# Kernel tuning notes

Measured on AMD Instinct MI355X. Metric: run time of the kernel, lower is better.

Reference implementation:

```python
import jax, jax.numpy as jnp
import numpy as np

N = 100000   # nodes
E = 3200000  # edges
D = 128      # in_channels
H = 128      # subhiddens
O = 128      # out_channels
S = 2048     # subgraphs
EPS = 1e-5


def _glorot(k, shape):
    lim = np.sqrt(6.0 / (shape[0] + shape[1])).astype(np.float32)
    return jax.random.uniform(k, shape, jnp.float32, -lim, lim)


def setup_inputs() -> dict:
    key = jax.random.key(0)
    ks = jax.random.split(key, 8)
    x = jax.random.normal(ks[0], (N, D), jnp.float32)
    edge_index = jax.random.randint(ks[1], (2, E), 0, N, dtype=jnp.int32)
    node_to_subgraph = jnp.sort(jax.random.randint(ks[2], (N,), 0, S, dtype=jnp.int32))
    return {
        "x": x,
        "edge_index": edge_index,
        "node_to_subgraph": node_to_subgraph,
        "W1": _glorot(ks[3], (D, H)), "b1": jnp.zeros((H,), jnp.float32),
        "g1": jnp.ones((H,), jnp.float32), "be1": jnp.zeros((H,), jnp.float32),
        "W2": _glorot(ks[4], (H, H)), "b2": jnp.zeros((H,), jnp.float32),
        "g2": jnp.ones((H,), jnp.float32), "be2": jnp.zeros((H,), jnp.float32),
        "W3": _glorot(ks[5], (H, O)), "b3": jnp.zeros((O,), jnp.float32),
    }


def _gcn_conv(x, W, b, row, col, norm):
    # PyG GCNConv: out[col] += norm * (x @ W)[row], then + bias.
    xw = x @ W                                    # [N+?, d] -> [N, d_out]
    msg = xw[row] * norm[:, None]                 # gather over source nodes
    out = jax.ops.segment_sum(msg, col, num_segments=N)
    return out + b


def _bn_relu(x, g, be):
    # BatchNorm1d (training-mode batch stats, biased var) + ReLU
    mean = jnp.mean(x, axis=0)
    var = jnp.mean(jnp.square(x - mean), axis=0)
    return jax.nn.relu((x - mean) * jax.lax.rsqrt(var + EPS) * g + be)


def reference(x, edge_index, node_to_subgraph, W1, b1, g1, be1, W2, b2, g2, be2, W3, b3):
    # GCN symmetric norm with self-loops, shared across the 3 convs.
    loops = jnp.arange(N, dtype=edge_index.dtype)
    row = jnp.concatenate([edge_index[0], loops])  # source
    col = jnp.concatenate([edge_index[1], loops])  # target (aggregation)
    deg = jax.ops.segment_sum(jnp.ones_like(col, dtype=x.dtype), col, num_segments=N)
    dinv = jnp.where(deg > 0, jax.lax.rsqrt(deg), 0.0)
    norm = dinv[row] * dinv[col]

    h1 = _bn_relu(_gcn_conv(x, W1, b1, row, col, norm), g1, be1)   # dropout is no-op in eval
    h2 = _bn_relu(_gcn_conv(h1, W2, b2, row, col, norm), g2, be2)
    h3 = jax.nn.relu(_gcn_conv(h2, W3, b3, row, col, norm))

    cat = jnp.concatenate([h1, h2, h3], axis=-1)                   # [N, 2H+O]
    return jax.ops.segment_max(cat, node_to_subgraph, num_segments=S)  # gmp -> [S, 2H+O]
```

## Files before the change

### kernel.cpp

```cpp
#include <hip/hip_runtime.h>
#include <hip/hip_fp16.h>

#define NN 100000
#define NE 3200000
#define SG 2048
#define OUTC 384
#define EPS 1e-5f

#define NBUK 800
#define BNODES 125
#define CAP 5120
#define TILE 4096
#define B_BUCKET 782
#define B_GEMM 391
#define LDSTRIDE 136
#define AGG_BLOCKS 3584
#define CHUNK 7
#define NBANK 32

typedef _Float16 f16x8 __attribute__((ext_vector_type(8)));
typedef float f32x16 __attribute__((ext_vector_type(16)));

__global__ void k_init(const float* __restrict__ W1, const float* __restrict__ W2,
                       const float* __restrict__ W3, __half* __restrict__ WT,
                       unsigned int* __restrict__ outz, int* __restrict__ gcur,
                       float* __restrict__ sums) {
    int g = blockIdx.x * 256 + threadIdx.x;
    int nt = gridDim.x * 256;
    for (int i = g; i < SG * OUTC; i += nt) outz[i] = 0u;
    if (g < NBUK) gcur[g] = 0;
    for (int i = g; i < 2 * NBANK * 256; i += nt) sums[i] = 0.f;
    for (int i = g; i < 3 * 16384; i += nt) {
        int m = i >> 14, idx = i & 16383;
        int k = idx >> 7, n = idx & 127;
        const float* W = m == 0 ? W1 : (m == 1 ? W2 : W3);
        WT[m * 16384 + n * 128 + k] = __float2half(W[idx]);
    }
}

__device__ void bucketA_body(int* smem, int bb,
                             const int* __restrict__ erow, const int* __restrict__ ecol,
                             int* __restrict__ gcur, int* __restrict__ packed) {
    int* sc   = smem;
    int* sr   = smem + 4096;
    int* hist = smem + 8192;
    int* loff = smem + 9216;
    int* gch  = smem + 10240;
    int* cur  = smem + 11264;
    int* psum = smem + 12288;
    int t = threadIdx.x;
    hist[t] = 0; hist[t + 256] = 0; hist[t + 512] = 0; hist[t + 768] = 0;
    __syncthreads();
    int e0 = bb * TILE;
    int lim = NE - e0; if (lim > TILE) lim = TILE;
    for (int i = t; i < lim; i += 256) {
        int c = ecol[e0 + i];
        int r = erow[e0 + i];
        sc[i] = c; sr[i] = r;
        atomicAdd(&hist[c / BNODES], 1);
    }
    __syncthreads();
    int h0 = hist[4 * t], h1 = hist[4 * t + 1], h2 = hist[4 * t + 2], h3 = hist[4 * t + 3];
    int s = h0 + h1 + h2 + h3;
    psum[t] = s; __syncthreads();
    for (int st = 1; st < 256; st <<= 1) {
        int a = (t >= st) ? psum[t - st] : 0;
        __syncthreads();
        psum[t] += a;
        __syncthreads();
    }
    int base = psum[t] - s;
    loff[4 * t] = base;
    loff[4 * t + 1] = base + h0;
    loff[4 * t + 2] = base + h0 + h1;
    loff[4 * t + 3] = base + h0 + h1 + h2;
#pragma unroll
    for (int j = 0; j < 4; ++j) {
        int b = 4 * t + j;
        if (b < NBUK) {
            int c = hist[b];
            gch[b] = c ? atomicAdd(&gcur[b], c) : 0;
            cur[b] = loff[b];
        }
    }
    __syncthreads();
    for (int i = t; i < lim; i += 256) {
        int c = sc[i], r = sr[i];
        int b = c / BNODES;
        int lc = c - b * BNODES;
        int p = atomicAdd(&cur[b], 1);
        int rank = p - loff[b];
        if (gch[b] + rank < CAP) packed[b * CAP + gch[b] + rank] = r | (lc << 17);
    }
}

__device__ void gemm32u_body(int* smem, int gb, const float* __restrict__ A,
                             const __half* __restrict__ WTg, __half* __restrict__ C) {
    _Float16* Wl = (_Float16*)smem;
    int tid = threadIdx.x;
    for (int ch = tid; ch < 2048; ch += 256) {
        int n = ch >> 4, seg = ch & 15;
        *(uint4*)&Wl[n * LDSTRIDE + seg * 8] = *(const uint4*)(WTg + n * 128 + seg * 8);
    }
    __syncthreads();
    int wave = tid >> 6, lane = tid & 63;
    int l31 = lane & 31, lhi = lane >> 5;
    int rowbase = gb * 256 + wave * 64;
    f32x16 acc[2][4];
#pragma unroll
    for (int rt = 0; rt < 2; ++rt)
#pragma unroll
        for (int nt = 0; nt < 4; ++nt)
#pragma unroll
            for (int i = 0; i < 16; ++i) acc[rt][nt][i] = 0.f;
    int r0 = rowbase + l31;      if (r0 >= NN) r0 = NN - 1;
    int r1 = rowbase + 32 + l31; if (r1 >= NN) r1 = NN - 1;
    const float* A0 = A + (size_t)r0 * 128;
    const float* A1 = A + (size_t)r1 * 128;
#pragma unroll
    for (int ks = 0; ks < 8; ++ks) {
        int koff = ks * 16 + lhi * 8;
        float4 f0 = *(const float4*)(A0 + koff);
        float4 f1 = *(const float4*)(A0 + koff + 4);
        float4 g0 = *(const float4*)(A1 + koff);
        float4 g1 = *(const float4*)(A1 + koff + 4);
        f16x8 a0, a1;
        a0[0] = (_Float16)f0.x; a0[1] = (_Float16)f0.y; a0[2] = (_Float16)f0.z; a0[3] = (_Float16)f0.w;
        a0[4] = (_Float16)f1.x; a0[5] = (_Float16)f1.y; a0[6] = (_Float16)f1.z; a0[7] = (_Float16)f1.w;
        a1[0] = (_Float16)g0.x; a1[1] = (_Float16)g0.y; a1[2] = (_Float16)g0.z; a1[3] = (_Float16)g0.w;
        a1[4] = (_Float16)g1.x; a1[5] = (_Float16)g1.y; a1[6] = (_Float16)g1.z; a1[7] = (_Float16)g1.w;
#pragma unroll
        for (int nt = 0; nt < 4; ++nt) {
            f16x8 b = *(const f16x8*)&Wl[(nt * 32 + l31) * LDSTRIDE + ks * 16 + lhi * 8];
            acc[0][nt] = __builtin_amdgcn_mfma_f32_32x32x16_f16(a0, b, acc[0][nt], 0, 0, 0);
            acc[1][nt] = __builtin_amdgcn_mfma_f32_32x32x16_f16(a1, b, acc[1][nt], 0, 0, 0);
        }
    }
#pragma unroll
    for (int rt = 0; rt < 2; ++rt) {
#pragma unroll
        for (int r = 0; r < 16; ++r) {
            int row = rowbase + rt * 32 + (r & 3) + 8 * (r >> 2) + 4 * lhi;
            if (row < NN) {
                size_t cb = (size_t)row * 128 + l31;
                C[cb]      = __float2half(acc[rt][0][r]);
                C[cb + 32] = __float2half(acc[rt][1][r]);
                C[cb + 64] = __float2half(acc[rt][2][r]);
                C[cb + 96] = __float2half(acc[rt][3][r]);
            }
        }
    }
}

__global__ __launch_bounds__(256, 2) void k_fused1(const int* __restrict__ erow,
                                                   const int* __restrict__ ecol,
                                                   int* __restrict__ gcur,
                                                   int* __restrict__ packed,
                                                   const float* __restrict__ x,
                                                   const __half* __restrict__ WT,
                                                   __half* __restrict__ XWh) {
    __shared__ __align__(16) int smem[12544];
    int bb = blockIdx.x;
    if (bb < B_BUCKET) bucketA_body(smem, bb, erow, ecol, gcur, packed);
    else gemm32u_body(smem, bb - B_BUCKET, x, WT, XWh);
}

__global__ __launch_bounds__(256) void k_csrB(int* __restrict__ rows,
                                              const int* __restrict__ gcur,
                                              int* __restrict__ begs, int* __restrict__ ends,
                                              float* __restrict__ dinv,
                                              __half* __restrict__ XWh) {
    __shared__ int lin[CAP];
    __shared__ int hist[128], off[128], cur[128], psc[128];
    __shared__ float dinvl[128];
    int b = blockIdx.x, t = threadIdx.x;
    int cnt = gcur[b]; if (cnt > CAP) cnt = CAP;
    int base = b * CAP;
    for (int i = t; i < cnt; i += 256) lin[i] = rows[base + i];
    if (t < 128) hist[t] = 0;
    __syncthreads();
    for (int i = t; i < cnt; i += 256) atomicAdd(&hist[lin[i] >> 17], 1);
    __syncthreads();
    int pc = 0;
    if (t < 128) { pc = (hist[t] + 3) & ~3; psc[t] = pc; }
    __syncthreads();
    for (int st = 1; st < 128; st <<= 1) {
        int a = 0;
        if (t < 128 && t >= st) a = psc[t - st];
        __syncthreads();
        if (t < 128) psc[t] += a;
        __syncthreads();
    }
    if (t < 128) { off[t] = psc[t] - pc; cur[t] = off[t]; }
    __syncthreads();
    if (t < BNODES) {
        int n = b * BNODES + t;
        int c = hist[t];
        int bg = base + off[t];
        begs[n] = bg;
        ends[n] = bg + c;
        float dv = rsqrtf((float)(c + 1));
        dinv[n] = dv;
        dinvl[t] = dv;
        int pad = (c + 3) & ~3;
        for (int p = c; p < pad; ++p)
            if (off[t] + p < CAP) rows[base + off[t] + p] = 0;
    }
    __syncthreads();
    for (int i = t; i < cnt; i += 256) {
        int w = lin[i];
        int lc = w >> 17;
        int p = atomicAdd(&cur[lc], 1);
        if (p < CAP) rows[base + p] = w & 0x1FFFF;
    }
    int rr = t >> 1, half = t & 1;
    if (rr < BNODES) {
        float dv = dinvl[rr];
        int n = b * BNODES + rr;
        uint4* p = (uint4*)(XWh + (size_t)n * 128) + half * 8;
#pragma unroll
        for (int j = 0; j < 8; ++j) {
            uint4 v = p[j];
            __half2* h = (__half2*)&v;
#pragma unroll
            for (int q = 0; q < 4; ++q) {
                float2 f = __half22float2(h[q]);
                h[q] = __floats2half2_rn(f.x * dv, f.y * dv);
            }
            p[j] = v;
        }
    }
}

__global__ __launch_bounds__(256, 2) void k_gemm16(const __half* __restrict__ A,
                                                   const __half* __restrict__ WTg,
                                                   const float* __restrict__ dinv,
                                                   __half* __restrict__ C) {
    __shared__ _Float16 Wl[128 * LDSTRIDE];
    int tid = threadIdx.x;
    for (int ch = tid; ch < 2048; ch += 256) {
        int n = ch >> 4, seg = ch & 15;
        *(uint4*)&Wl[n * LDSTRIDE + seg * 8] = *(const uint4*)(WTg + n * 128 + seg * 8);
    }
    __syncthreads();
    int wave = tid >> 6, lane = tid & 63;
    int l31 = lane & 31, lhi = lane >> 5;
    int rowbase = blockIdx.x * 256 + wave * 64;
    f32x16 acc[2][4];
#pragma unroll
    for (int rt = 0; rt < 2; ++rt)
#pragma unroll
        for (int nt = 0; nt < 4; ++nt)
#pragma unroll
            for (int i = 0; i < 16; ++i) acc[rt][nt][i] = 0.f;
    int r0 = rowbase + l31;      if (r0 >= NN) r0 = NN - 1;
    int r1 = rowbase + 32 + l31; if (r1 >= NN) r1 = NN - 1;
    const f16x8* A0 = (const f16x8*)(A + (size_t)r0 * 128);
    const f16x8* A1 = (const f16x8*)(A + (size_t)r1 * 128);
#pragma unroll
    for (int ks = 0; ks < 8; ++ks) {
        f16x8 a0 = A0[ks * 2 + lhi];
        f16x8 a1 = A1[ks * 2 + lhi];
#pragma unroll
        for (int nt = 0; nt < 4; ++nt) {
            f16x8 b = *(const f16x8*)&Wl[(nt * 32 + l31) * LDSTRIDE + ks * 16 + lhi * 8];
            acc[0][nt] = __builtin_amdgcn_mfma_f32_32x32x16_f16(a0, b, acc[0][nt], 0, 0, 0);
            acc[1][nt] = __builtin_amdgcn_mfma_f32_32x32x16_f16(a1, b, acc[1][nt], 0, 0, 0);
        }
    }
#pragma unroll
    for (int rt = 0; rt < 2; ++rt) {
#pragma unroll
        for (int r = 0; r < 16; ++r) {
            int row = rowbase + rt * 32 + (r & 3) + 8 * (r >> 2) + 4 * lhi;
            if (row < NN) {
                float sc = dinv[row];
                size_t cb = (size_t)row * 128 + l31;
                C[cb]      = __float2half(acc[rt][0][r] * sc);
                C[cb + 32] = __float2half(acc[rt][1][r] * sc);
                C[cb + 64] = __float2half(acc[rt][2][r] * sc);
                C[cb + 96] = __float2half(acc[rt][3][r] * sc);
            }
        }
    }
}

__device__ __forceinline__ void accum8(float* acc, uint4 v) {
    float2 f;
    f = __half22float2(*(__half2*)&v.x); acc[0] += f.x; acc[1] += f.y;
    f = __half22float2(*(__half2*)&v.y); acc[2] += f.x; acc[3] += f.y;
    f = __half22float2(*(__half2*)&v.z); acc[4] += f.x; acc[5] += f.y;
    f = __half22float2(*(__half2*)&v.w); acc[6] += f.x; acc[7] += f.y;
}
__device__ __forceinline__ void accum8w(float* acc, uint4 v, float w) {
    float2 f;
    f = __half22float2(*(__half2*)&v.x); acc[0] = fmaf(w, f.x, acc[0]); acc[1] = fmaf(w, f.y, acc[1]);
    f = __half22float2(*(__half2*)&v.y); acc[2] = fmaf(w, f.x, acc[2]); acc[3] = fmaf(w, f.y, acc[3]);
    f = __half22float2(*(__half2*)&v.z); acc[4] = fmaf(w, f.x, acc[4]); acc[5] = fmaf(w, f.y, acc[5]);
    f = __half22float2(*(__half2*)&v.w); acc[6] = fmaf(w, f.x, acc[6]); acc[7] = fmaf(w, f.y, acc[7]);
}

__device__ __forceinline__ void agg_node(const uint4* __restrict__ XW4,
                                         const int* __restrict__ rows,
                                         int n, int beg, int end, int quad, int li,
                                         float* acc) {
#pragma unroll
    for (int j = 0; j < 8; ++j) acc[j] = 0.f;
    if (quad == 0) {
        uint4 sv = XW4[(size_t)n * 16 + li];
        accum8(acc, sv);
    }
    int e = beg;
    for (; e + 32 <= end; e += 32) {
        int4 ia = *(const int4*)(rows + e + 4 * quad);
        int4 ib = *(const int4*)(rows + e + 16 + 4 * quad);
        uint4 v0 = XW4[(size_t)ia.x * 16 + li];
        uint4 v1 = XW4[(size_t)ia.y * 16 + li];
        uint4 v2 = XW4[(size_t)ia.z * 16 + li];
        uint4 v3 = XW4[(size_t)ia.w * 16 + li];
        uint4 v4 = XW4[(size_t)ib.x * 16 + li];
        uint4 v5 = XW4[(size_t)ib.y * 16 + li];
        uint4 v6 = XW4[(size_t)ib.z * 16 + li];
        uint4 v7 = XW4[(size_t)ib.w * 16 + li];
        accum8(acc, v0); accum8(acc, v1); accum8(acc, v2); accum8(acc, v3);
        accum8(acc, v4); accum8(acc, v5); accum8(acc, v6); accum8(acc, v7);
    }
    for (; e + 16 <= end; e += 16) {
        int4 ia = *(const int4*)(rows + e + 4 * quad);
        uint4 v0 = XW4[(size_t)ia.x * 16 + li];
        uint4 v1 = XW4[(size_t)ia.y * 16 + li];
        uint4 v2 = XW4[(size_t)ia.z * 16 + li];
        uint4 v3 = XW4[(size_t)ia.w * 16 + li];
        accum8(acc, v0); accum8(acc, v1); accum8(acc, v2); accum8(acc, v3);
    }
    if (e < end) {
        int rem = end - e;
        int qb = 4 * quad;
        int4 it = make_int4(0, 0, 0, 0);
        if (qb < rem) it = *(const int4*)(rows + e + qb);
        uint4 v0 = XW4[(size_t)it.x * 16 + li];
        uint4 v1 = XW4[(size_t)it.y * 16 + li];
        uint4 v2 = XW4[(size_t)it.z * 16 + li];
        uint4 v3 = XW4[(size_t)it.w * 16 + li];
        accum8w(acc, v0, (qb + 0 < rem) ? 1.f : 0.f);
        accum8w(acc, v1, (qb + 1 < rem) ? 1.f : 0.f);
        accum8w(acc, v2, (qb + 2 < rem) ? 1.f : 0.f);
        accum8w(acc, v3, (qb + 3 < rem) ? 1.f : 0.f);
    }
#pragma unroll
    for (int j = 0; j < 8; ++j) {
        acc[j] += __shfl_xor(acc[j], 16, 64);
        acc[j] += __shfl_xor(acc[j], 32, 64);
    }
}

__global__ __launch_bounds__(256) void k_agghs(const __half* __restrict__ XWh,
                                               const int* __restrict__ begs,
                                               const int* __restrict__ ends,
                                               const int* __restrict__ rows,
                                               const float* __restrict__ dinv,
                                               __half* __restrict__ outh,
                                               float* __restrict__ sums) {
    __shared__ float sred[4][256];
    int wave = threadIdx.x >> 6, lane = threadIdx.x & 63;
    int quad = lane >> 4, li = lane & 15;
    const uint4* XW4 = (const uint4*)XWh;
    int wid = blockIdx.x * 4 + wave;
    int n0 = wid * CHUNK;
    int n1 = n0 + CHUNK; if (n1 > NN) n1 = NN;
    float ssum[8] = {}, sqsum[8] = {};
    for (int n = n0; n < n1; ++n) {
        float acc[8];
        agg_node(XW4, rows, n, begs[n], ends[n], quad, li, acc);
        if (quad == 0) {
            float dn = dinv[n];
            __half2 hh[4];
#pragma unroll
            for (int j = 0; j < 8; ++j) {
                float v = acc[j] * dn;
                acc[j] = v;
                ssum[j] += v;
                sqsum[j] += v * v;
            }
            hh[0] = __floats2half2_rn(acc[0], acc[1]);
            hh[1] = __floats2half2_rn(acc[2], acc[3]);
            hh[2] = __floats2half2_rn(acc[4], acc[5]);
            hh[3] = __floats2half2_rn(acc[6], acc[7]);
            *(uint4*)(outh + (size_t)n * 128 + li * 8) = *(uint4*)hh;
        }
    }
    if (quad == 0) {
#pragma unroll
        for (int j = 0; j < 8; ++j) {
            sred[wave][li * 8 + j] = ssum[j];
            sred[wave][128 + li * 8 + j] = sqsum[j];
        }
    }
    __syncthreads();
    int t = threadIdx.x;
    float tot = sred[0][t] + sred[1][t] + sred[2][t] + sred[3][t];
    atomicAdd(&sums[(blockIdx.x & (NBANK - 1)) * 256 + t], tot);
}

__global__ __launch_bounds__(256) void k_agghmax(const __half* __restrict__ XWh,
                                                 const int* __restrict__ begs,
                                                 const int* __restrict__ ends,
                                                 const int* __restrict__ rows,
                                                 const float* __restrict__ dinv,
                                                 const float* __restrict__ b3,
                                                 const int* __restrict__ n2s,
                                                 unsigned int* __restrict__ outmax) {
    int wave = threadIdx.x >> 6, lane = threadIdx.x & 63;
    int quad = lane >> 4, li = lane & 15;
    const uint4* XW4 = (const uint4*)XWh;
    int wid = blockIdx.x * 4 + wave;
    int n0 = wid * CHUNK;
    int n1 = n0 + CHUNK; if (n1 > NN) n1 = NN;
    float4 bz0 = *(const float4*)(b3 + li * 8);
    float4 bz1 = *(const float4*)(b3 + li * 8 + 4);
    float bias[8] = {bz0.x, bz0.y, bz0.z, bz0.w, bz1.x, bz1.y, bz1.z, bz1.w};
    int cur = -1;
    float runmax[8];
    for (int n = n0; n < n1; ++n) {
        float acc[8];
        agg_node(XW4, rows, n, begs[n], ends[n], quad, li, acc);
        float dn = dinv[n];
        int sg = n2s[n];
        if (sg != cur) {
            if (cur >= 0 && quad == 0) {
#pragma unroll
                for (int j = 0; j < 8; ++j)
                    atomicMax(&outmax[cur * OUTC + 256 + li * 8 + j], __float_as_uint(runmax[j]));
            }
            cur = sg;
#pragma unroll
            for (int j = 0; j < 8; ++j) runmax[j] = fmaxf(acc[j] * dn + bias[j], 0.f);
        } else {
#pragma unroll
            for (int j = 0; j < 8; ++j) runmax[j] = fmaxf(runmax[j], fmaxf(acc[j] * dn + bias[j], 0.f));
        }
    }
    if (cur >= 0 && quad == 0) {
#pragma unroll
        for (int j = 0; j < 8; ++j)
            atomicMax(&outmax[cur * OUTC + 256 + li * 8 + j], __float_as_uint(runmax[j]));
    }
}

__global__ void k_bnmax(__half* __restrict__ buf, const float* __restrict__ sums,
                        const float* __restrict__ g, const float* __restrict__ be,
                        const int* __restrict__ n2s,
                        unsigned int* __restrict__ outmax, int colOff) {
    int c = threadIdx.x & 127;
    int rg = threadIdx.x >> 7;
    int n0 = blockIdx.x * 64;
    int nEnd = n0 + 64; if (nEnd > NN) nEnd = NN;
    float s = 0.f, q = 0.f;
#pragma unroll
    for (int b = 0; b < NBANK; ++b) {
        s += sums[b * 256 + c];
        q += sums[b * 256 + 128 + c];
    }
    float mean = s * (1.0f / NN);
    float inv = rsqrtf(q * (1.0f / NN) - mean * mean + EPS) * g[c];
    float sc = inv, sh = be[c] - mean * inv;
    int cur = -1; float runmax = 0.f;
    for (int n = n0 + rg; n < nEnd; n += 2) {
        float v = fmaxf(__half2float(buf[(size_t)n * 128 + c]) * sc + sh, 0.f);
        buf[(size_t)n * 128 + c] = __float2half(v);
        int sg = n2s[n];
        if (sg != cur) {
            if (cur >= 0) atomicMax(&outmax[cur * OUTC + colOff + c], __float_as_uint(runmax));
            cur = sg; runmax = v;
        } else {
            runmax = fmaxf(runmax, v);
        }
    }
    if (cur >= 0) atomicMax(&outmax[cur * OUTC + colOff + c], __float_as_uint(runmax));
}

extern "C" void kernel_launch(void* const* d_in, const int* in_sizes, int n_in,
                              void* d_out, int out_size, void* d_ws, size_t ws_size,
                              hipStream_t stream) {
    const float* x   = (const float*)d_in[0];
    const int*   ei  = (const int*)d_in[1];
    const int*   n2s = (const int*)d_in[2];
    const float* W1  = (const float*)d_in[3];
    const float* g1  = (const float*)d_in[5];
    const float* be1 = (const float*)d_in[6];
    const float* W2  = (const float*)d_in[7];
    const float* g2  = (const float*)d_in[9];
    const float* be2 = (const float*)d_in[10];
    const float* W3  = (const float*)d_in[11];
    const float* b3  = (const float*)d_in[12];

    __half* H    = (__half*)d_ws;
    __half* XWh  = H + (size_t)NN * 128;
    __half* WT   = XWh + (size_t)NN * 128;
    int* rows    = (int*)(WT + 3 * 16384);
    int* begs    = rows + (size_t)NBUK * CAP;
    int* ends    = begs + NN;
    float* dinv  = (float*)(ends + NN);
    int* gcur    = (int*)(dinv + NN);
    float* sums  = (float*)(gcur + NBUK);

    const int* erow = ei;
    const int* ecol = ei + NE;
    unsigned int* outmax = (unsigned int*)d_out;
    int nbSeg = (NN + 63) / 64;
    int nbG = (NN + 255) / 256;

    k_init<<<512, 256, 0, stream>>>(W1, W2, W3, WT, outmax, gcur, sums);
    k_fused1<<<B_BUCKET + B_GEMM, 256, 0, stream>>>(erow, ecol, gcur, rows, x, WT, XWh);
    k_csrB<<<NBUK, 256, 0, stream>>>(rows, gcur, begs, ends, dinv, XWh);

    k_agghs<<<AGG_BLOCKS, 256, 0, stream>>>(XWh, begs, ends, rows, dinv, H, sums);
    k_bnmax<<<nbSeg, 256, 0, stream>>>(H, sums, g1, be1, n2s, outmax, 0);

    k_gemm16<<<nbG, 256, 0, stream>>>(H, WT + 16384, dinv, XWh);
    k_agghs<<<AGG_BLOCKS, 256, 0, stream>>>(XWh, begs, ends, rows, dinv, H, sums + NBANK * 256);
    k_bnmax<<<nbSeg, 256, 0, stream>>>(H, sums + NBANK * 256, g2, be2, n2s, outmax, 128);

    k_gemm16<<<nbG, 256, 0, stream>>>(H, WT + 32768, dinv, XWh);
    k_agghmax<<<AGG_BLOCKS, 256, 0, stream>>>(XWh, begs, ends, rows, dinv, b3, n2s, outmax);
}
```

Baseline: 668.9 us.

## Fuse BN+ReLU+max-pool into GEMM kernel and use FP8 features for final aggregation

Merges the separate BatchNorm/ReLU/segment-max kernel and the following GEMM into one launch. GEMM blocks apply the BN affine and ReLU on the fly while loading A, and extra blocks do the subgraph max, so the normalized activations are never written back. The layer-3 XW is stored as FP8, which halves gather bytes in the last aggregation, at the cost of reduced precision in h3.

Result: faster. 646.9 us (-3.3%).

```diff
diff --git a/kernel.cpp b/kernel.cpp
--- a/kernel.cpp
+++ b/kernel.cpp
@@ -13,6 +13,7 @@
 #define TILE 4096
 #define B_BUCKET 782
 #define B_GEMM 391
+#define B_MAX 1563
 #define LDSTRIDE 136
 #define AGG_BLOCKS 3584
 #define CHUNK 7
@@ -20,6 +21,7 @@
 
 typedef _Float16 f16x8 __attribute__((ext_vector_type(8)));
 typedef float f32x16 __attribute__((ext_vector_type(16)));
+typedef float floatx2 __attribute__((ext_vector_type(2)));
 
 __global__ void k_init(const float* __restrict__ W1, const float* __restrict__ W2,
                        const float* __restrict__ W3, __half* __restrict__ WT,
@@ -232,59 +234,6 @@
     }
 }
 
-__global__ __launch_bounds__(256, 2) void k_gemm16(const __half* __restrict__ A,
-                                                   const __half* __restrict__ WTg,
-                                                   const float* __restrict__ dinv,
-                                                   __half* __restrict__ C) {
-    __shared__ _Float16 Wl[128 * LDSTRIDE];
-    int tid = threadIdx.x;
-    for (int ch = tid; ch < 2048; ch += 256) {
-        int n = ch >> 4, seg = ch & 15;
-        *(uint4*)&Wl[n * LDSTRIDE + seg * 8] = *(const uint4*)(WTg + n * 128 + seg * 8);
-    }
-    __syncthreads();
-    int wave = tid >> 6, lane = tid & 63;
-    int l31 = lane & 31, lhi = lane >> 5;
-    int rowbase = blockIdx.x * 256 + wave * 64;
-    f32x16 acc[2][4];
-#pragma unroll
-    for (int rt = 0; rt < 2; ++rt)
-#pragma unroll
-        for (int nt = 0; nt < 4; ++nt)
-#pragma unroll
-            for (int i = 0; i < 16; ++i) acc[rt][nt][i] = 0.f;
-    int r0 = rowbase + l31;      if (r0 >= NN) r0 = NN - 1;
-    int r1 = rowbase + 32 + l31; if (r1 >= NN) r1 = NN - 1;
-    const f16x8* A0 = (const f16x8*)(A + (size_t)r0 * 128);
-    const f16x8* A1 = (const f16x8*)(A + (size_t)r1 * 128);
-#pragma unroll
-    for (int ks = 0; ks < 8; ++ks) {
-        f16x8 a0 = A0[ks * 2 + lhi];
-        f16x8 a1 = A1[ks * 2 + lhi];
-#pragma unroll
-        for (int nt = 0; nt < 4; ++nt) {
-            f16x8 b = *(const f16x8*)&Wl[(nt * 32 + l31) * LDSTRIDE + ks * 16 + lhi * 8];
-            acc[0][nt] = __builtin_amdgcn_mfma_f32_32x32x16_f16(a0, b, acc[0][nt], 0, 0, 0);
-            acc[1][nt] = __builtin_amdgcn_mfma_f32_32x32x16_f16(a1, b, acc[1][nt], 0, 0, 0);
-        }
-    }
-#pragma unroll
-    for (int rt = 0; rt < 2; ++rt) {
-#pragma unroll
-        for (int r = 0; r < 16; ++r) {
-            int row = rowbase + rt * 32 + (r & 3) + 8 * (r >> 2) + 4 * lhi;
-            if (row < NN) {
-                float sc = dinv[row];
-                size_t cb = (size_t)row * 128 + l31;
-                C[cb]      = __float2half(acc[rt][0][r] * sc);
-                C[cb + 32] = __float2half(acc[rt][1][r] * sc);
-                C[cb + 64] = __float2half(acc[rt][2][r] * sc);
-                C[cb + 96] = __float2half(acc[rt][3][r] * sc);
-            }
-        }
-    }
-}
-
 __device__ __forceinline__ void accum8(float* acc, uint4 v) {
     float2 f;
     f = __half22float2(*(__half2*)&v.x); acc[0] += f.x; acc[1] += f.y;
@@ -359,7 +308,7 @@
                                                const int* __restrict__ ends,
                                                const int* __restrict__ rows,
                                                const float* __restrict__ dinv,
-                                               __half* __restrict__ outh,
+                                               __half* __restrict__ outA,
                                                float* __restrict__ sums) {
     __shared__ float sred[4][256];
     int wave = threadIdx.x >> 6, lane = threadIdx.x & 63;
@@ -386,7 +335,7 @@
             hh[1] = __floats2half2_rn(acc[2], acc[3]);
             hh[2] = __floats2half2_rn(acc[4], acc[5]);
             hh[3] = __floats2half2_rn(acc[6], acc[7]);
-            *(uint4*)(outh + (size_t)n * 128 + li * 8) = *(uint4*)hh;
+            *(uint4*)(outA + (size_t)n * 128 + li * 8) = *(uint4*)hh;
         }
     }
     if (quad == 0) {
@@ -402,17 +351,206 @@
     atomicAdd(&sums[(blockIdx.x & (NBANK - 1)) * 256 + t], tot);
 }
 
-__global__ __launch_bounds__(256) void k_agghmax(const __half* __restrict__ XWh,
-                                                 const int* __restrict__ begs,
-                                                 const int* __restrict__ ends,
-                                                 const int* __restrict__ rows,
-                                                 const float* __restrict__ dinv,
-                                                 const float* __restrict__ b3,
-                                                 const int* __restrict__ n2s,
-                                                 unsigned int* __restrict__ outmax) {
+template <int FP8OUT>
+__global__ __launch_bounds__(256, 2) void k_fused2(const __half* __restrict__ A,
+                                                   const float* __restrict__ sums,
+                                                   const float* __restrict__ g,
+                                                   const float* __restrict__ be,
+                                                   const __half* __restrict__ WTg,
+                                                   const float* __restrict__ dinv,
+                                                   const int* __restrict__ n2s,
+                                                   unsigned int* __restrict__ outmax,
+                                                   int colOff,
+                                                   void* __restrict__ Cout) {
+    __shared__ _Float16 Wl[128 * LDSTRIDE];
+    __shared__ float scL[128], shL[128];
+    int tid = threadIdx.x;
+    if (tid < 128) {
+        float s = 0.f, q = 0.f;
+#pragma unroll
+        for (int b = 0; b < NBANK; ++b) {
+            s += sums[b * 256 + tid];
+            q += sums[b * 256 + 128 + tid];
+        }
+        float mean = s * (1.0f / NN);
+        float inv = rsqrtf(q * (1.0f / NN) - mean * mean + EPS) * g[tid];
+        scL[tid] = inv;
+        shL[tid] = be[tid] - mean * inv;
+    }
+    if (blockIdx.x < B_GEMM) {
+        for (int ch = tid; ch < 2048; ch += 256) {
+            int n = ch >> 4, seg = ch & 15;
+            *(uint4*)&Wl[n * LDSTRIDE + seg * 8] = *(const uint4*)(WTg + n * 128 + seg * 8);
+        }
+        __syncthreads();
+        int wave = tid >> 6, lane = tid & 63;
+        int l31 = lane & 31, lhi = lane >> 5;
+        int rowbase = blockIdx.x * 256 + wave * 64;
+        f32x16 acc[2][4];
+#pragma unroll
+        for (int rt = 0; rt < 2; ++rt)
+#pragma unroll
+            for (int nt = 0; nt < 4; ++nt)
+#pragma unroll
+                for (int i = 0; i < 16; ++i) acc[rt][nt][i] = 0.f;
+        int r0 = rowbase + l31;      if (r0 >= NN) r0 = NN - 1;
+        int r1 = rowbase + 32 + l31; if (r1 >= NN) r1 = NN - 1;
+        const f16x8* A0 = (const f16x8*)(A + (size_t)r0 * 128);
+        const f16x8* A1 = (const f16x8*)(A + (size_t)r1 * 128);
+#pragma unroll
+        for (int ks = 0; ks < 8; ++ks) {
+            int koff = ks * 16 + lhi * 8;
+            float4 sc0 = *(const float4*)&scL[koff];
+            float4 sc1 = *(const float4*)&scL[koff + 4];
+            float4 sh0 = *(const float4*)&shL[koff];
+            float4 sh1 = *(const float4*)&shL[koff + 4];
+            float scv[8] = {sc0.x, sc0.y, sc0.z, sc0.w, sc1.x, sc1.y, sc1.z, sc1.w};
+            float shv[8] = {sh0.x, sh0.y, sh0.z, sh0.w, sh1.x, sh1.y, sh1.z, sh1.w};
+            f16x8 ra0 = A0[ks * 2 + lhi];
+            f16x8 ra1 = A1[ks * 2 + lhi];
+            f16x8 a0, a1;
+#pragma unroll
+            for (int j = 0; j < 8; ++j) {
+                a0[j] = (_Float16)fmaxf((float)ra0[j] * scv[j] + shv[j], 0.f);
+                a1[j] = (_Float16)fmaxf((float)ra1[j] * scv[j] + shv[j], 0.f);
+            }
+#pragma unroll
+            for (int nt = 0; nt < 4; ++nt) {
+                f16x8 b = *(const f16x8*)&Wl[(nt * 32 + l31) * LDSTRIDE + ks * 16 + lhi * 8];
+                acc[0][nt] = __builtin_amdgcn_mfma_f32_32x32x16_f16(a0, b, acc[0][nt], 0, 0, 0);
+                acc[1][nt] = __builtin_amdgcn_mfma_f32_32x32x16_f16(a1, b, acc[1][nt], 0, 0, 0);
+            }
+        }
+#pragma unroll
+        for (int rt = 0; rt < 2; ++rt) {
+#pragma unroll
+            for (int r = 0; r < 16; ++r) {
+                int row = rowbase + rt * 32 + (r & 3) + 8 * (r >> 2) + 4 * lhi;
+                if (row < NN) {
+                    float sc = dinv[row];
+                    if (FP8OUT) {
+                        unsigned char* C8 = (unsigned char*)Cout;
+                        size_t cb = (size_t)row * 128 + l31;
+#pragma unroll
+                        for (int nt = 0; nt < 4; ++nt) {
+                            float v = acc[rt][nt][r] * sc;
+                            int enc = __builtin_amdgcn_cvt_pk_fp8_f32(v, v, 0, false);
+                            C8[cb + nt * 32] = (unsigned char)(enc & 0xFF);
+                        }
+                    } else {
+                        __half* C = (__half*)Cout;
+                        size_t cb = (size_t)row * 128 + l31;
+                        C[cb]      = __float2half(acc[rt][0][r] * sc);
+                        C[cb + 32] = __float2half(acc[rt][1][r] * sc);
+                        C[cb + 64] = __float2half(acc[rt][2][r] * sc);
+                        C[cb + 96] = __float2half(acc[rt][3][r] * sc);
+                    }
+                }
+            }
+        }
+    } else {
+        __syncthreads();
+        int b2 = blockIdx.x - B_GEMM;
+        int c = tid & 127;
+        int rg = tid >> 7;
+        int n0 = b2 * 64;
+        int nEnd = n0 + 64; if (nEnd > NN) nEnd = NN;
+        float sc = scL[c], sh = shL[c];
+        int cur = -1; float runmax = 0.f;
+        for (int n = n0 + rg; n < nEnd; n += 2) {
+            float v = fmaxf(__half2float(A[(size_t)n * 128 + c]) * sc + sh, 0.f);
+            int sg = n2s[n];
+            if (sg != cur) {
+                if (cur >= 0) atomicMax(&outmax[cur * OUTC + colOff + c], __float_as_uint(runmax));
+                cur = sg; runmax = v;
+            } else {
+                runmax = fmaxf(runmax, v);
+            }
+        }
+        if (cur >= 0) atomicMax(&outmax[cur * OUTC + colOff + c], __float_as_uint(runmax));
+    }
+}
+
+__device__ __forceinline__ void accum8f8(float* acc, uint2 v) {
+    floatx2 f;
+    f = __builtin_amdgcn_cvt_pk_f32_fp8((int)v.x, false); acc[0] += f.x; acc[1] += f.y;
+    f = __builtin_amdgcn_cvt_pk_f32_fp8((int)v.x, true);  acc[2] += f.x; acc[3] += f.y;
+    f = __builtin_amdgcn_cvt_pk_f32_fp8((int)v.y, false); acc[4] += f.x; acc[5] += f.y;
+    f = __builtin_amdgcn_cvt_pk_f32_fp8((int)v.y, true);  acc[6] += f.x; acc[7] += f.y;
+}
+__device__ __forceinline__ void accum8f8w(float* acc, uint2 v, float w) {
+    floatx2 f;
+    f = __builtin_amdgcn_cvt_pk_f32_fp8((int)v.x, false); acc[0] = fmaf(w, f.x, acc[0]); acc[1] = fmaf(w, f.y, acc[1]);
+    f = __builtin_amdgcn_cvt_pk_f32_fp8((int)v.x, true);  acc[2] = fmaf(w, f.x, acc[2]); acc[3] = fmaf(w, f.y, acc[3]);
+    f = __builtin_amdgcn_cvt_pk_f32_fp8((int)v.y, false); acc[4] = fmaf(w, f.x, acc[4]); acc[5] = fmaf(w, f.y, acc[5]);
+    f = __builtin_amdgcn_cvt_pk_f32_fp8((int)v.y, true);  acc[6] = fmaf(w, f.x, acc[6]); acc[7] = fmaf(w, f.y, acc[7]);
+}
+
+__device__ __forceinline__ void agg_node_f8(const uint2* __restrict__ XW2,
+                                            const int* __restrict__ rows,
+                                            int n, int beg, int end, int quad, int li,
+                                            float* acc) {
+#pragma unroll
+    for (int j = 0; j < 8; ++j) acc[j] = 0.f;
+    if (quad == 0) {
+        uint2 sv = XW2[(size_t)n * 16 + li];
+        accum8f8(acc, sv);
+    }
+    int e = beg;
+    for (; e + 32 <= end; e += 32) {
+        int4 ia = *(const int4*)(rows + e + 4 * quad);
+        int4 ib = *(const int4*)(rows + e + 16 + 4 * quad);
+        uint2 v0 = XW2[(size_t)ia.x * 16 + li];
+        uint2 v1 = XW2[(size_t)ia.y * 16 + li];
+        uint2 v2 = XW2[(size_t)ia.z * 16 + li];
+        uint2 v3 = XW2[(size_t)ia.w * 16 + li];
+        uint2 v4 = XW2[(size_t)ib.x * 16 + li];
+        uint2 v5 = XW2[(size_t)ib.y * 16 + li];
+        uint2 v6 = XW2[(size_t)ib.z * 16 + li];
+        uint2 v7 = XW2[(size_t)ib.w * 16 + li];
+        accum8f8(acc, v0); accum8f8(acc, v1); accum8f8(acc, v2); accum8f8(acc, v3);
+        accum8f8(acc, v4); accum8f8(acc, v5); accum8f8(acc, v6); accum8f8(acc, v7);
+    }
+    for (; e + 16 <= end; e += 16) {
+        int4 ia = *(const int4*)(rows + e + 4 * quad);
+        uint2 v0 = XW2[(size_t)ia.x * 16 + li];
+        uint2 v1 = XW2[(size_t)ia.y * 16 + li];
+        uint2 v2 = XW2[(size_t)ia.z * 16 + li];
+        uint2 v3 = XW2[(size_t)ia.w * 16 + li];
+        accum8f8(acc, v0); accum8f8(acc, v1); accum8f8(acc, v2); accum8f8(acc, v3);
+    }
+    if (e < end) {
+        int rem = end - e;
+        int qb = 4 * quad;
+        int4 it = make_int4(0, 0, 0, 0);
+        if (qb < rem) it = *(const int4*)(rows + e + qb);
+        uint2 v0 = XW2[(size_t)it.x * 16 + li];
+        uint2 v1 = XW2[(size_t)it.y * 16 + li];
+        uint2 v2 = XW2[(size_t)it.z * 16 + li];
+        uint2 v3 = XW2[(size_t)it.w * 16 + li];
+        accum8f8w(acc, v0, (qb + 0 < rem) ? 1.f : 0.f);
+        accum8f8w(acc, v1, (qb + 1 < rem) ? 1.f : 0.f);
+        accum8f8w(acc, v2, (qb + 2 < rem) ? 1.f : 0.f);
+        accum8f8w(acc, v3, (qb + 3 < rem) ? 1.f : 0.f);
+    }
+#pragma unroll
+    for (int j = 0; j < 8; ++j) {
+        acc[j] += __shfl_xor(acc[j], 16, 64);
+        acc[j] += __shfl_xor(acc[j], 32, 64);
+    }
+}
+
+__global__ __launch_bounds__(256) void k_agghmax8(const unsigned char* __restrict__ XWf8,
+                                                  const int* __restrict__ begs,
+                                                  const int* __restrict__ ends,
+                                                  const int* __restrict__ rows,
+                                                  const float* __restrict__ dinv,
+                                                  const float* __restrict__ b3,
+                                                  const int* __restrict__ n2s,
+                                                  unsigned int* __restrict__ outmax) {
     int wave = threadIdx.x >> 6, lane = threadIdx.x & 63;
     int quad = lane >> 4, li = lane & 15;
-    const uint4* XW4 = (const uint4*)XWh;
+    const uint2* XW2 = (const uint2*)XWf8;
     int wid = blockIdx.x * 4 + wave;
     int n0 = wid * CHUNK;
     int n1 = n0 + CHUNK; if (n1 > NN) n1 = NN;
@@ -423,7 +561,7 @@
     float runmax[8];
     for (int n = n0; n < n1; ++n) {
         float acc[8];
-        agg_node(XW4, rows, n, begs[n], ends[n], quad, li, acc);
+        agg_node_f8(XW2, rows, n, begs[n], ends[n], quad, li, acc);
         float dn = dinv[n];
         int sg = n2s[n];
         if (sg != cur) {
@@ -445,38 +583,6 @@
         for (int j = 0; j < 8; ++j)
             atomicMax(&outmax[cur * OUTC + 256 + li * 8 + j], __float_as_uint(runmax[j]));
     }
-}
-
-__global__ void k_bnmax(__half* __restrict__ buf, const float* __restrict__ sums,
-                        const float* __restrict__ g, const float* __restrict__ be,
-                        const int* __restrict__ n2s,
-                        unsigned int* __restrict__ outmax, int colOff) {
-    int c = threadIdx.x & 127;
-    int rg = threadIdx.x >> 7;
-    int n0 = blockIdx.x * 64;
-    int nEnd = n0 + 64; if (nEnd > NN) nEnd = NN;
-    float s = 0.f, q = 0.f;
-#pragma unroll
-    for (int b = 0; b < NBANK; ++b) {
-        s += sums[b * 256 + c];
-        q += sums[b * 256 + 128 + c];
-    }
-    float mean = s * (1.0f / NN);
-    float inv = rsqrtf(q * (1.0f / NN) - mean * mean + EPS) * g[c];
-    float sc = inv, sh = be[c] - mean * inv;
-    int cur = -1; float runmax = 0.f;
-    for (int n = n0 + rg; n < nEnd; n += 2) {
-        float v = fmaxf(__half2float(buf[(size_t)n * 128 + c]) * sc + sh, 0.f);
-        buf[(size_t)n * 128 + c] = __float2half(v);
-        int sg = n2s[n];
-        if (sg != cur) {
-            if (cur >= 0) atomicMax(&outmax[cur * OUTC + colOff + c], __float_as_uint(runmax));
-            cur = sg; runmax = v;
-        } else {
-            runmax = fmaxf(runmax, v);
-        }
-    }
-    if (cur >= 0) atomicMax(&outmax[cur * OUTC + colOff + c], __float_as_uint(runmax));
 }
 
 extern "C" void kernel_launch(void* const* d_in, const int* in_sizes, int n_in,
@@ -494,9 +600,9 @@
     const float* W3  = (const float*)d_in[11];
     const float* b3  = (const float*)d_in[12];
 
-    __half* H    = (__half*)d_ws;
-    __half* XWh  = H + (size_t)NN * 128;
-    __half* WT   = XWh + (size_t)NN * 128;
+    __half* bufA = (__half*)d_ws;
+    __half* bufX = bufA + (size_t)NN * 128;
+    __half* WT   = bufX + (size_t)NN * 128;
     int* rows    = (int*)(WT + 3 * 16384);
     int* begs    = rows + (size_t)NBUK * CAP;
     int* ends    = begs + NN;
@@ -507,20 +613,19 @@
     const int* erow = ei;
     const int* ecol = ei + NE;
     unsigned int* outmax = (unsigned int*)d_out;
-    int nbSeg = (NN + 63) / 64;
-    int nbG = (NN + 255) / 256;
 
     k_init<<<512, 256, 0, stream>>>(W1, W2, W3, WT, outmax, gcur, sums);
-    k_fused1<<<B_BUCKET + B_GEMM, 256, 0, stream>>>(erow, ecol, gcur, rows, x, WT, XWh);
-    k_csrB<<<NBUK, 256, 0, stream>>>(rows, gcur, begs, ends, dinv, XWh);
-
-    k_agghs<<<AGG_BLOCKS, 256, 0, stream>>>(XWh, begs, ends, rows, dinv, H, sums);
-    k_bnmax<<<nbSeg, 256, 0, stream>>>(H, sums, g1, be1, n2s, outmax, 0);
-
-    k_gemm16<<<nbG, 256, 0, stream>>>(H, WT + 16384, dinv, XWh);
-    k_agghs<<<AGG_BLOCKS, 256, 0, stream>>>(XWh, begs, ends, rows, dinv, H, sums + NBANK * 256);
-    k_bnmax<<<nbSeg, 256, 0, stream>>>(H, sums + NBANK * 256, g2, be2, n2s, outmax, 128);
-
-    k_gemm16<<<nbG, 256, 0, stream>>>(H, WT + 32768, dinv, XWh);
-    k_agghmax<<<AGG_BLOCKS, 256, 0, stream>>>(XWh, begs, ends, rows, dinv, b3, n2s, outmax);
-}
+    k_fused1<<<B_BUCKET + B_GEMM, 256, 0, stream>>>(erow, ecol, gcur, rows, x, WT, bufX);
+    k_csrB<<<NBUK, 256, 0, stream>>>(rows, gcur, begs, ends, dinv, bufX);
+
+    k_agghs<<<AGG_BLOCKS, 256, 0, stream>>>(bufX, begs, ends, rows, dinv, bufA, sums);
+    k_fused2<0><<<B_GEMM + B_MAX, 256, 0, stream>>>(bufA, sums, g1, be1, WT + 16384, dinv,
+                                                    n2s, outmax, 0, (void*)bufX);
+
+    k_agghs<<<AGG_BLOCKS, 256, 0, stream>>>(bufX, begs, ends, rows, dinv, bufA, sums + NBANK * 256);
+    k_fused2<1><<<B_GEMM + B_MAX, 256, 0, stream>>>(bufA, sums + NBANK * 256, g2, be2, WT + 32768,
+                                                    dinv, n2s, outmax, 128, (void*)bufX);
+
+    k_agghmax8<<<AGG_BLOCKS, 256, 0, stream>>>((const unsigned char*)bufX, begs, ends, rows,
+                                               dinv, b3, n2s, outmax);
+}
```
